# Kernel optimization log

Measured on AMD Instinct MI355X. Metric: run time of the kernel, lower is better.

Reference implementation:

```python
import jax, jax.numpy as jnp
import numpy as np

D_MODEL = 1024
N_HEADS = 16
D_H = D_MODEL // N_HEADS
B, S = 2, 2048


def setup_inputs() -> dict:
    key = jax.random.key(0)
    ks = jax.random.split(key, 12)
    s = 1.0 / np.sqrt(D_MODEL)
    inp = {
        "Q": jax.random.normal(ks[0], (B, S, D_MODEL), jnp.float32),
        "K": jax.random.normal(ks[1], (B, S, D_MODEL), jnp.float32),
        "V": jax.random.normal(ks[2], (B, S, D_MODEL), jnp.float32),
        # causal mask: True means masked out (matches masked_fill semantics)
        "masked": jnp.broadcast_to(~jnp.tril(jnp.ones((S, S), bool)), (B, S, S)),
        "WQ_w": jax.random.uniform(ks[3], (D_MODEL, D_MODEL), jnp.float32, -s, s),
        "WQ_b": jax.random.uniform(ks[4], (D_MODEL,), jnp.float32, -s, s),
        "WK_w": jax.random.uniform(ks[5], (D_MODEL, D_MODEL), jnp.float32, -s, s),
        "WK_b": jax.random.uniform(ks[6], (D_MODEL,), jnp.float32, -s, s),
        "WV_w": jax.random.uniform(ks[7], (D_MODEL, D_MODEL), jnp.float32, -s, s),
        "WV_b": jax.random.uniform(ks[8], (D_MODEL,), jnp.float32, -s, s),
        "Wo_w": jax.random.uniform(ks[9], (D_MODEL, D_MODEL), jnp.float32, -s, s),
        "Wo_b": jax.random.uniform(ks[10], (D_MODEL,), jnp.float32, -s, s),
    }
    return inp


def reference(Q, K, V, masked, WQ_w, WQ_b, WK_w, WK_b, WV_w, WV_b, Wo_w, Wo_b):
    b = Q.shape[0]
    # torch Linear: y = x @ W^T + b
    def split_heads(x):
        return x.reshape(b, -1, N_HEADS, D_H).transpose(0, 2, 1, 3)  # [B,H,S,d_h]

    q = split_heads(Q @ WQ_w.T + WQ_b)
    k = split_heads(K @ WK_w.T + WK_b)
    v = split_heads(V @ WV_w.T + WV_b)

    scores = jnp.einsum("bhqd,bhkd->bhqk", q, k) / np.sqrt(D_H)
    scores = jnp.where(masked[:, None, :, :], jnp.float32(-1e9), scores)
    attn = jax.nn.softmax(scores, axis=-1)
    ctx = jnp.einsum("bhqk,bhkd->bhqd", attn, v)  # [B,H,S,d_h]
    ctx = ctx.transpose(0, 2, 1, 3).reshape(b, -1, N_HEADS * D_H)
    return ctx @ Wo_w.T + Wo_b
```

## Files before the change

### kernel.cpp

```cpp
#include <hip/hip_runtime.h>
#include <hip/hip_bf16.h>
#include <math.h>


typedef __bf16 bf16_t;
typedef bf16_t bf16x8 __attribute__((ext_vector_type(8)));
typedef bf16_t bf16x4 __attribute__((ext_vector_type(4)));
typedef float f32x4 __attribute__((ext_vector_type(4)));

#define MFMA16(a, b, c) __builtin_amdgcn_mfma_f32_16x16x32_bf16(a, b, c, 0, 0, 0)

constexpr int S_LEN = 2048;
constexpr int DMODEL = 1024;
constexpr int DHEAD = 64;
constexpr int MTOT = 2 * S_LEN;
constexpr size_t NQ = (size_t)MTOT * DMODEL;
constexpr size_t NW = (size_t)DMODEL * DMODEL;
constexpr float ESC = 0.18033688011112042f;

__device__ __forceinline__ void load_lds16(const void* g, void* l) {
  __builtin_amdgcn_global_load_lds((const __attribute__((address_space(1))) void*)g,
                                   (__attribute__((address_space(3))) void*)l, 16, 0, 0);
}

__device__ __forceinline__ void swap32(unsigned& a, unsigned& b) {
#if __has_builtin(__builtin_amdgcn_permlane32_swap)
  auto r = __builtin_amdgcn_permlane32_swap(a, b, false, false);
  a = r[0]; b = r[1];
#else
  asm volatile("s_nop 1\n\tv_permlane32_swap_b32 %0, %1\n\ts_nop 1"
               : "+v"(a), "+v"(b));
#endif
}
__device__ __forceinline__ void swap16(unsigned& a, unsigned& b) {
#if __has_builtin(__builtin_amdgcn_permlane16_swap)
  auto r = __builtin_amdgcn_permlane16_swap(a, b, false, false);
  a = r[0]; b = r[1];
#else
  asm volatile("s_nop 1\n\tv_permlane16_swap_b32 %0, %1\n\ts_nop 1"
               : "+v"(a), "+v"(b));
#endif
}

__device__ __forceinline__ float fexp2(float x) {
#if __has_builtin(__builtin_amdgcn_exp2f)
  return __builtin_amdgcn_exp2f(x);
#else
  float r;
  asm("v_exp_f32 %0, %1\n\ts_nop 1" : "=v"(r) : "v"(x));
  return r;
#endif
}

__global__ __launch_bounds__(256) void convert_all(
    const float* __restrict__ Q, const float* __restrict__ K, const float* __restrict__ V,
    const float* __restrict__ W0, const float* __restrict__ W1, const float* __restrict__ W2,
    const float* __restrict__ W3, bf16_t* __restrict__ dst) {
  const size_t i = ((size_t)blockIdx.x * 256 + threadIdx.x) * 4;
  const float* s;
  size_t off = i;
  if (off < NQ) { s = Q; }
  else if (off < 2 * NQ) { s = K; off -= NQ; }
  else if (off < 3 * NQ) { s = V; off -= 2 * NQ; }
  else {
    off -= 3 * NQ;
    if (off < NW) { s = W0; }
    else if (off < 2 * NW) { s = W1; off -= NW; }
    else if (off < 3 * NW) { s = W2; off -= 2 * NW; }
    else { s = W3; off -= 3 * NW; }
  }
  const float4 v4 = *(const float4*)(s + off);
  bf16x4 b;
  b[0] = (bf16_t)v4.x; b[1] = (bf16_t)v4.y; b[2] = (bf16_t)v4.z; b[3] = (bf16_t)v4.w;
  *(bf16x4*)(dst + i) = b;
}

template <int BK>
__device__ __forceinline__ void gemm_loop(const bf16_t* __restrict__ Ab,
                                          const bf16_t* __restrict__ Wb,
                                          bf16_t* As, bf16_t* Ws,
                                          f32x4 (&acc)[4][4], int wave, int lane) {
  constexpr int CH = BK / 8;
  constexpr int RPI = 64 / CH;
  constexpr int IPW = BK / 16;
  const int col = lane & 15, quad = lane >> 4;
  const int wm = (wave >> 1) * 64, wn = (wave & 1) * 64;
  const int srow = lane / CH;
  const int sch = lane % CH;

  for (int k0 = 0; k0 < 1024; k0 += BK) {
    __syncthreads();
#pragma unroll
    for (int i = 0; i < IPW; i++) {
      const int rbase = (i * 4 + wave) * RPI;
      const int g = sch ^ ((rbase + srow) & 7);
      load_lds16(Ab + (size_t)(rbase + srow) * 1024 + k0 + g * 8, As + rbase * BK);
      load_lds16(Wb + (size_t)(rbase + srow) * 1024 + k0 + g * 8, Ws + rbase * BK);
    }
    __syncthreads();
#pragma unroll
    for (int kc = 0; kc < BK / 32; kc++) {
      const int slot = (kc * 4 + quad) ^ (col & 7);
      bf16x8 af[4], wf[4];
#pragma unroll
      for (int i = 0; i < 4; i++) af[i] = *(const bf16x8*)&As[(wm + i * 16 + col) * BK + slot * 8];
#pragma unroll
      for (int j = 0; j < 4; j++) wf[j] = *(const bf16x8*)&Ws[(wn + j * 16 + col) * BK + slot * 8];
#pragma unroll
      for (int i = 0; i < 4; i++)
#pragma unroll
        for (int j = 0; j < 4; j++) acc[i][j] = MFMA16(af[i], wf[j], acc[i][j]);
    }
  }
}

__global__ __launch_bounds__(256, 3) void gemm_qkv(const bf16_t* __restrict__ Abase,
                                                   const bf16_t* __restrict__ Wbase,
                                                   const float* __restrict__ b0,
                                                   const float* __restrict__ b1,
                                                   const float* __restrict__ b2,
                                                   bf16_t* __restrict__ obase) {
  __shared__ bf16_t As[128 * 64];
  __shared__ bf16_t Ws[128 * 64];
  const int z = blockIdx.z;
  const int bm = blockIdx.x * 128, bn = blockIdx.y * 128;
  const int lane = threadIdx.x & 63, wave = threadIdx.x >> 6;
  const int col = lane & 15, quad = lane >> 4;
  const int wm = (wave >> 1) * 64, wn = (wave & 1) * 64;

  f32x4 acc[4][4];
#pragma unroll
  for (int i = 0; i < 4; i++)
#pragma unroll
    for (int j = 0; j < 4; j++)
#pragma unroll
      for (int r = 0; r < 4; r++) acc[i][j][r] = 0.f;

  const bf16_t* A = Abase + z * NQ + (size_t)bm * 1024;
  const bf16_t* W = Wbase + z * NW + (size_t)bn * 1024;
  const float* bias = (z == 0) ? b0 : ((z == 1) ? b1 : b2);
  bf16_t* out = obase + z * NQ;

  gemm_loop<64>(A, W, As, Ws, acc, wave, lane);

  const float esc = (z == 0) ? ESC : 1.0f;
#pragma unroll
  for (int i = 0; i < 4; i++) {
#pragma unroll
    for (int j = 0; j < 4; j++) {
      const int n = bn + wn + j * 16 + col;
      const float bv = bias[n];
      const int h = n >> 6, dh = n & 63;
      if (z < 2) {
#pragma unroll
        for (int r = 0; r < 4; r++) {
          const int m = bm + wm + i * 16 + quad * 4 + r;
          const int b = m >> 11, s = m & 2047;
          out[((size_t)((b * 16 + h) * S_LEN + s) << 6) | dh] =
              (bf16_t)((acc[i][j][r] + bv) * esc);
        }
      } else {
        const int m0 = bm + wm + i * 16 + quad * 4;
        const int b = m0 >> 11, s0 = m0 & 2047;
        bf16x4 p4;
#pragma unroll
        for (int r = 0; r < 4; r++) p4[r] = (bf16_t)(acc[i][j][r] + bv);
        *(bf16x4*)&out[(((size_t)((b * 16 + h) * DHEAD + dh)) << 11) | s0] = p4;
      }
    }
  }
}

__global__ __launch_bounds__(256, 2) void gemm_out(const bf16_t* __restrict__ A,
                                                   const bf16_t* __restrict__ W,
                                                   const float* __restrict__ bias,
                                                   float* __restrict__ out) {
  __shared__ bf16_t As[64 * 64];
  __shared__ bf16_t Ws[128 * 64];
  const int bm = blockIdx.x * 64, bn = blockIdx.y * 128;
  const int lane = threadIdx.x & 63, wave = threadIdx.x >> 6;
  const int col = lane & 15, quad = lane >> 4;
  const int wm = (wave >> 1) * 32, wn = (wave & 1) * 64;

  f32x4 acc[2][4];
#pragma unroll
  for (int i = 0; i < 2; i++)
#pragma unroll
    for (int j = 0; j < 4; j++)
#pragma unroll
      for (int r = 0; r < 4; r++) acc[i][j][r] = 0.f;

  const int srow = lane >> 3, s7 = lane & 7;
  const bf16_t* Ab = A + (size_t)bm * 1024;
  const bf16_t* Wb = W + (size_t)bn * 1024;

  for (int k0 = 0; k0 < 1024; k0 += 64) {
    __syncthreads();
#pragma unroll
    for (int i = 0; i < 2; i++) {
      const int rbase = (i * 4 + wave) * 8;
      const int g = s7 ^ srow;
      load_lds16(Ab + (size_t)(rbase + srow) * 1024 + k0 + g * 8, As + rbase * 64);
    }
#pragma unroll
    for (int i = 0; i < 4; i++) {
      const int rbase = (i * 4 + wave) * 8;
      const int g = s7 ^ srow;
      load_lds16(Wb + (size_t)(rbase + srow) * 1024 + k0 + g * 8, Ws + rbase * 64);
    }
    __syncthreads();
#pragma unroll
    for (int kc = 0; kc < 2; kc++) {
      const int slot = (kc * 4 + quad) ^ (col & 7);
      bf16x8 af[2], wf[4];
#pragma unroll
      for (int i = 0; i < 2; i++) af[i] = *(const bf16x8*)&As[(wm + i * 16 + col) * 64 + slot * 8];
#pragma unroll
      for (int j = 0; j < 4; j++) wf[j] = *(const bf16x8*)&Ws[(wn + j * 16 + col) * 64 + slot * 8];
#pragma unroll
      for (int i = 0; i < 2; i++)
#pragma unroll
        for (int j = 0; j < 4; j++) acc[i][j] = MFMA16(af[i], wf[j], acc[i][j]);
    }
  }

#pragma unroll
  for (int i = 0; i < 2; i++)
#pragma unroll
    for (int j = 0; j < 4; j++) {
      const int n = bn + wn + j * 16 + col;
      const float bv = bias[n];
#pragma unroll
      for (int r = 0; r < 4; r++) {
        const int m = bm + wm + i * 16 + quad * 4 + r;
        out[(size_t)m * DMODEL + n] = acc[i][j][r] + bv;
      }
    }
}

__global__ __launch_bounds__(256, 2) void attn(const bf16_t* __restrict__ q,
                                               const bf16_t* __restrict__ k,
                                               const bf16_t* __restrict__ vT,
                                               bf16_t* __restrict__ ctx) {
  const int bh = blockIdx.x;
  const int y = blockIdx.y;
  const int T = (y < 8) ? (15 - y) : (y - 8);
  const int cmax = 2 * T + 1;
  const int lane = threadIdx.x & 63, wave = threadIdx.x >> 6;
  const int col = lane & 15, quad = lane >> 4;
  const int qrel = wave * 16 + col;

  __shared__ bf16_t Ks[2][64 * 64];
  __shared__ bf16_t Vs[2][64 * 64];

  const bf16_t* kbh = k + (size_t)bh * S_LEN * DHEAD;
  const bf16_t* vbh = vT + (size_t)bh * DHEAD * S_LEN;

  const int srow8 = lane >> 3, s7 = lane & 7;
  const int g8 = s7 ^ srow8;

  auto stage = [&](int c, int b) {
#pragma unroll
    for (int i = 0; i < 2; i++) {
      const int rbase = (i * 4 + wave) * 8;
      load_lds16(kbh + (size_t)(c * 64 + rbase + srow8) * DHEAD + g8 * 8,
                 &Ks[b][rbase * 64]);
    }
#pragma unroll
    for (int i = 0; i < 2; i++) {
      const int dbase = (i * 4 + wave) * 8;
      load_lds16(vbh + (size_t)(dbase + srow8) * S_LEN + c * 64 + g8 * 8,
                 &Vs[b][dbase * 64]);
    }
  };

  const bf16_t* qb0 = q + ((size_t)bh * S_LEN + T * 128 + qrel) * DHEAD;
  bf16x8 aq[2][2];
  aq[0][0] = *(const bf16x8*)(qb0 + quad * 8);
  aq[0][1] = *(const bf16x8*)(qb0 + 32 + quad * 8);
  aq[1][0] = *(const bf16x8*)(qb0 + (size_t)64 * DHEAD + quad * 8);
  aq[1][1] = *(const bf16x8*)(qb0 + (size_t)64 * DHEAD + 32 + quad * 8);

  f32x4 o0[4], o1[4], lacc0, lacc1;
#pragma unroll
  for (int db = 0; db < 4; db++)
#pragma unroll
    for (int r = 0; r < 4; r++) { o0[db][r] = 0.f; o1[db][r] = 0.f; }
#pragma unroll
  for (int r = 0; r < 4; r++) { lacc0[r] = 0.f; lacc1[r] = 0.f; }
  const f32x4 Zv = {0.f, 0.f, 0.f, 0.f};

  auto expw = [&](const f32x4& sv, int nb, bool dmask, f32x4& lac,
                  unsigned& w0, unsigned& w1) {
    union { bf16x4 v; unsigned u[2]; } pw;
#pragma unroll
    for (int r = 0; r < 4; r++) {
      float pv = fexp2(sv[r]);
      if (dmask && (nb * 16 + quad * 4 + r) > qrel) pv = 0.f;
      lac[r] += pv;
      pw.v[r] = (bf16_t)pv;
    }
    w0 = pw.u[0]; w1 = pw.u[1];
  };

  stage(0, 0);
  int buf = 0;

  for (int c = 0; c <= cmax; ++c) {
    __syncthreads();
    if (c < cmax) stage(c + 1, buf ^ 1);

    const bool skip0 = (c == cmax);
    const bool mask0 = (c == cmax - 1);
    const bool mask1 = (c == cmax);

    f32x4 s0[4], s1[4];
    {
      const int sl = quad ^ (col & 7);
      bf16x8 kf[4];
#pragma unroll
      for (int nb = 0; nb < 4; nb++)
        kf[nb] = *(const bf16x8*)&Ks[buf][(nb * 16 + col) * 64 + sl * 8];
      __builtin_amdgcn_s_setprio(1);
      if (!skip0) {
#pragma unroll
        for (int nb = 0; nb < 4; nb++) s0[nb] = MFMA16(kf[nb], aq[0][0], Zv);
      }
#pragma unroll
      for (int nb = 0; nb < 4; nb++) s1[nb] = MFMA16(kf[nb], aq[1][0], Zv);
      __builtin_amdgcn_s_setprio(0);
    }
    {
      const int sl = (4 + quad) ^ (col & 7);
      bf16x8 kf[4];
#pragma unroll
      for (int nb = 0; nb < 4; nb++)
        kf[nb] = *(const bf16x8*)&Ks[buf][(nb * 16 + col) * 64 + sl * 8];
      __builtin_amdgcn_s_setprio(1);
      if (!skip0) {
#pragma unroll
        for (int nb = 0; nb < 4; nb++) s0[nb] = MFMA16(kf[nb], aq[0][1], s0[nb]);
      }
#pragma unroll
      for (int nb = 0; nb < 4; nb++) s1[nb] = MFMA16(kf[nb], aq[1][1], s1[nb]);
      __builtin_amdgcn_s_setprio(0);
    }

#pragma unroll
    for (int kcp = 0; kcp < 2; kcp++) {
      const int sl = (kcp * 4 + quad) ^ (col & 7);
      bf16x8 bv[4];
#pragma unroll
      for (int db = 0; db < 4; db++)
        bv[db] = *(const bf16x8*)&Vs[buf][(db * 16 + col) * 64 + sl * 8];

      union { unsigned u[4]; bf16x8 v; } pa1, pa0;
      {
        unsigned X0, X1, Y0, Y1;
        expw(s1[2 * kcp], 2 * kcp, mask1, lacc1, X0, X1);
        expw(s1[2 * kcp + 1], 2 * kcp + 1, mask1, lacc1, Y0, Y1);
        swap32(X0, Y0); swap16(X0, Y0);
        swap32(X1, Y1); swap16(X1, Y1);
        pa1.u[0] = X0; pa1.u[1] = X1; pa1.u[2] = Y0; pa1.u[3] = Y1;
      }
      if (!skip0) {
        unsigned X0, X1, Y0, Y1;
        expw(s0[2 * kcp], 2 * kcp, mask0, lacc0, X0, X1);
        expw(s0[2 * kcp + 1], 2 * kcp + 1, mask0, lacc0, Y0, Y1);
        swap32(X0, Y0); swap16(X0, Y0);
        swap32(X1, Y1); swap16(X1, Y1);
        pa0.u[0] = X0; pa0.u[1] = X1; pa0.u[2] = Y0; pa0.u[3] = Y1;
      }
      __builtin_amdgcn_s_setprio(1);
      if (!skip0) {
#pragma unroll
        for (int db = 0; db < 4; db++) o0[db] = MFMA16(bv[db], pa0.v, o0[db]);
      }
#pragma unroll
      for (int db = 0; db < 4; db++) o1[db] = MFMA16(bv[db], pa1.v, o1[db]);
      __builtin_amdgcn_s_setprio(0);
    }
    buf ^= 1;
  }

  float l0 = lacc0[0] + lacc0[1] + lacc0[2] + lacc0[3];
  l0 += __shfl_xor(l0, 16); l0 += __shfl_xor(l0, 32);
  float l1 = lacc1[0] + lacc1[1] + lacc1[2] + lacc1[3];
  l1 += __shfl_xor(l1, 16); l1 += __shfl_xor(l1, 32);
  const float inv0 = 1.f / l0, inv1 = 1.f / l1;
  const int b = bh >> 4, h = bh & 15;
  bf16_t* cb0 = ctx + ((size_t)(b * S_LEN + T * 128 + qrel)) * DMODEL + h * DHEAD;
  bf16_t* cb1 = cb0 + (size_t)64 * DMODEL;
#pragma unroll
  for (int db = 0; db < 4; db++) {
    bf16x4 w0, w1;
#pragma unroll
    for (int r = 0; r < 4; r++) {
      w0[r] = (bf16_t)(o0[db][r] * inv0);
      w1[r] = (bf16_t)(o1[db][r] * inv1);
    }
    *(bf16x4*)&cb0[db * 16 + quad * 4] = w0;
    *(bf16x4*)&cb1[db * 16 + quad * 4] = w1;
  }
}

extern "C" void kernel_launch(void* const* d_in, const int* in_sizes, int n_in,
                              void* d_out, int out_size, void* d_ws, size_t ws_size,
                              hipStream_t stream) {
  const float* Q = (const float*)d_in[0];
  const float* K = (const float*)d_in[1];
  const float* V = (const float*)d_in[2];
  const float* WQw = (const float*)d_in[4];
  const float* WQb = (const float*)d_in[5];
  const float* WKw = (const float*)d_in[6];
  const float* WKb = (const float*)d_in[7];
  const float* WVw = (const float*)d_in[8];
  const float* WVb = (const float*)d_in[9];
  const float* Wow = (const float*)d_in[10];
  const float* Wob = (const float*)d_in[11];

  bf16_t* base = (bf16_t*)d_ws;
  bf16_t* Wc = base + 3 * NQ;
  bf16_t* qp = base + 3 * NQ + 4 * NW;
  bf16_t* ctx = base;

  const size_t total = 3 * NQ + 4 * NW;
  convert_all<<<dim3((unsigned)(total / 4 / 256)), dim3(256), 0, stream>>>(
      Q, K, V, WQw, WKw, WVw, Wow, base);

  gemm_qkv<<<dim3(32, 8, 3), dim3(256), 0, stream>>>(base, Wc, WQb, WKb, WVb, qp);
  attn<<<dim3(32, 16), dim3(256), 0, stream>>>(qp, qp + NQ, qp + 2 * NQ, ctx);
  gemm_out<<<dim3(64, 8), dim3(256), 0, stream>>>(ctx, Wc + 3 * NW, Wob, (float*)d_out);
}
```

Baseline: 233.9 us.

## Balance causal attention by pairing query tiles and splitting across two blocks

```diff
diff --git a/kernel.cpp b/kernel.cpp
--- a/kernel.cpp
+++ b/kernel.cpp
@@ -241,11 +241,15 @@
 __global__ __launch_bounds__(256, 2) void attn(const bf16_t* __restrict__ q,
                                                const bf16_t* __restrict__ k,
                                                const bf16_t* __restrict__ vT,
-                                               bf16_t* __restrict__ ctx) {
+                                               bf16_t* __restrict__ ctx,
+                                               float* __restrict__ pO,
+                                               float* __restrict__ pL) {
   const int bh = blockIdx.x;
-  const int y = blockIdx.y;
-  const int T = (y < 8) ? (15 - y) : (y - 8);
-  const int cmax = 2 * T + 1;
+  const int p = blockIdx.y;
+  const int s = blockIdx.z;
+  const int tB = 15 - p;
+  const int nA = s ? 0 : (2 * p + 2);
+  const int cB0 = s ? (15 - 2 * p) : 0;
   const int lane = threadIdx.x & 63, wave = threadIdx.x >> 6;
   const int col = lane & 15, quad = lane >> 4;
   const int qrel = wave * 16 + col;
@@ -274,20 +278,8 @@
     }
   };
 
-  const bf16_t* qb0 = q + ((size_t)bh * S_LEN + T * 128 + qrel) * DHEAD;
-  bf16x8 aq[2][2];
-  aq[0][0] = *(const bf16x8*)(qb0 + quad * 8);
-  aq[0][1] = *(const bf16x8*)(qb0 + 32 + quad * 8);
-  aq[1][0] = *(const bf16x8*)(qb0 + (size_t)64 * DHEAD + quad * 8);
-  aq[1][1] = *(const bf16x8*)(qb0 + (size_t)64 * DHEAD + 32 + quad * 8);
-
+  bf16x8 aqw[2][2];
   f32x4 o0[4], o1[4], lacc0, lacc1;
-#pragma unroll
-  for (int db = 0; db < 4; db++)
-#pragma unroll
-    for (int r = 0; r < 4; r++) { o0[db][r] = 0.f; o1[db][r] = 0.f; }
-#pragma unroll
-  for (int r = 0; r < 4; r++) { lacc0[r] = 0.f; lacc1[r] = 0.f; }
   const f32x4 Zv = {0.f, 0.f, 0.f, 0.f};
 
   auto expw = [&](const f32x4& sv, int nb, bool dmask, f32x4& lac,
@@ -303,16 +295,41 @@
     w0 = pw.u[0]; w1 = pw.u[1];
   };
 
-  stage(0, 0);
+  stage(cB0, 0);
   int buf = 0;
 
-  for (int c = 0; c <= cmax; ++c) {
+#pragma unroll 1
+  for (int i = 0; i < 17; ++i) {
+    const bool inB = (i >= nA);
+    const int c = inB ? (cB0 + i - nA) : i;
+    const int cm = inB ? (2 * tB + 1) : (2 * p + 1);
+
+    if (i == 0 || i == nA) {
+      const int tq = inB ? tB : p;
+      const bf16_t* qb = q + ((size_t)bh * S_LEN + tq * 128 + qrel) * DHEAD;
+      aqw[0][0] = *(const bf16x8*)(qb + quad * 8);
+      aqw[0][1] = *(const bf16x8*)(qb + 32 + quad * 8);
+      aqw[1][0] = *(const bf16x8*)(qb + (size_t)64 * DHEAD + quad * 8);
+      aqw[1][1] = *(const bf16x8*)(qb + (size_t)64 * DHEAD + 32 + quad * 8);
+#pragma unroll
+      for (int r = 0; r < 4; r++) { lacc0[r] = 0.f; lacc1[r] = 0.f; }
+#pragma unroll
+      for (int db = 0; db < 4; db++)
+#pragma unroll
+        for (int r = 0; r < 4; r++) { o0[db][r] = 0.f; o1[db][r] = 0.f; }
+    }
+
     __syncthreads();
-    if (c < cmax) stage(c + 1, buf ^ 1);
-
-    const bool skip0 = (c == cmax);
-    const bool mask0 = (c == cmax - 1);
-    const bool mask1 = (c == cmax);
+
+    if (i < 16) {
+      const int i1 = i + 1;
+      const int c1 = (i1 < nA) ? i1 : (cB0 + i1 - nA);
+      stage(c1, buf ^ 1);
+    }
+
+    const bool skip0 = (c == cm);
+    const bool mask0 = (c == cm - 1);
+    const bool mask1 = (c == cm);
 
     f32x4 s0[4], s1[4];
     {
@@ -324,10 +341,10 @@
       __builtin_amdgcn_s_setprio(1);
       if (!skip0) {
 #pragma unroll
-        for (int nb = 0; nb < 4; nb++) s0[nb] = MFMA16(kf[nb], aq[0][0], Zv);
-      }
-#pragma unroll
-      for (int nb = 0; nb < 4; nb++) s1[nb] = MFMA16(kf[nb], aq[1][0], Zv);
+        for (int nb = 0; nb < 4; nb++) s0[nb] = MFMA16(kf[nb], aqw[0][0], Zv);
+      }
+#pragma unroll
+      for (int nb = 0; nb < 4; nb++) s1[nb] = MFMA16(kf[nb], aqw[1][0], Zv);
       __builtin_amdgcn_s_setprio(0);
     }
     {
@@ -339,10 +356,10 @@
       __builtin_amdgcn_s_setprio(1);
       if (!skip0) {
 #pragma unroll
-        for (int nb = 0; nb < 4; nb++) s0[nb] = MFMA16(kf[nb], aq[0][1], s0[nb]);
-      }
-#pragma unroll
-      for (int nb = 0; nb < 4; nb++) s1[nb] = MFMA16(kf[nb], aq[1][1], s1[nb]);
+        for (int nb = 0; nb < 4; nb++) s0[nb] = MFMA16(kf[nb], aqw[0][1], s0[nb]);
+      }
+#pragma unroll
+      for (int nb = 0; nb < 4; nb++) s1[nb] = MFMA16(kf[nb], aqw[1][1], s1[nb]);
       __builtin_amdgcn_s_setprio(0);
     }
 
@@ -380,6 +397,28 @@
       for (int db = 0; db < 4; db++) o1[db] = MFMA16(bv[db], pa1.v, o1[db]);
       __builtin_amdgcn_s_setprio(0);
     }
+
+    if (i == nA - 1) {
+      float l0 = lacc0[0] + lacc0[1] + lacc0[2] + lacc0[3];
+      l0 += __shfl_xor(l0, 16); l0 += __shfl_xor(l0, 32);
+      float l1 = lacc1[0] + lacc1[1] + lacc1[2] + lacc1[3];
+      l1 += __shfl_xor(l1, 16); l1 += __shfl_xor(l1, 32);
+      const float inv0 = 1.f / l0, inv1 = 1.f / l1;
+      const int b = bh >> 4, h = bh & 15;
+      bf16_t* cb0 = ctx + ((size_t)(b * S_LEN + p * 128 + qrel)) * DMODEL + h * DHEAD;
+      bf16_t* cb1 = cb0 + (size_t)64 * DMODEL;
+#pragma unroll
+      for (int db = 0; db < 4; db++) {
+        bf16x4 w0, w1;
+#pragma unroll
+        for (int r = 0; r < 4; r++) {
+          w0[r] = (bf16_t)(o0[db][r] * inv0);
+          w1[r] = (bf16_t)(o1[db][r] * inv1);
+        }
+        *(bf16x4*)&cb0[db * 16 + quad * 4] = w0;
+        *(bf16x4*)&cb1[db * 16 + quad * 4] = w1;
+      }
+    }
     buf ^= 1;
   }
 
@@ -387,20 +426,39 @@
   l0 += __shfl_xor(l0, 16); l0 += __shfl_xor(l0, 32);
   float l1 = lacc1[0] + lacc1[1] + lacc1[2] + lacc1[3];
   l1 += __shfl_xor(l1, 16); l1 += __shfl_xor(l1, 32);
-  const float inv0 = 1.f / l0, inv1 = 1.f / l1;
+  const int slot = ((bh * 8 + p) << 1) | s;
+  float* myO = pO + (size_t)slot * (128 * 64);
+  float* myL = pL + slot * 128;
+#pragma unroll
+  for (int db = 0; db < 4; db++) {
+    *(f32x4*)&myO[(size_t)qrel * 64 + db * 16 + quad * 4] = o0[db];
+    *(f32x4*)&myO[(size_t)(64 + qrel) * 64 + db * 16 + quad * 4] = o1[db];
+  }
+  if (quad == 0) { myL[qrel] = l0; myL[64 + qrel] = l1; }
+}
+
+__global__ __launch_bounds__(256) void combine(const float* __restrict__ pO,
+                                               const float* __restrict__ pL,
+                                               bf16_t* __restrict__ ctx) {
+  const int pair = blockIdx.x;
+  const int bh = pair >> 3, p = pair & 7;
+  const int tB = 15 - p;
   const int b = bh >> 4, h = bh & 15;
-  bf16_t* cb0 = ctx + ((size_t)(b * S_LEN + T * 128 + qrel)) * DMODEL + h * DHEAD;
-  bf16_t* cb1 = cb0 + (size_t)64 * DMODEL;
-#pragma unroll
-  for (int db = 0; db < 4; db++) {
-    bf16x4 w0, w1;
-#pragma unroll
-    for (int r = 0; r < 4; r++) {
-      w0[r] = (bf16_t)(o0[db][r] * inv0);
-      w1[r] = (bf16_t)(o1[db][r] * inv1);
-    }
-    *(bf16x4*)&cb0[db * 16 + quad * 4] = w0;
-    *(bf16x4*)&cb1[db * 16 + quad * 4] = w1;
+  const float* O0 = pO + (size_t)(pair * 2 + 0) * (128 * 64);
+  const float* O1 = pO + (size_t)(pair * 2 + 1) * (128 * 64);
+  const float* L0 = pL + (pair * 2 + 0) * 128;
+  const float* L1 = pL + (pair * 2 + 1) * 128;
+#pragma unroll
+  for (int n = 0; n < 8; n++) {
+    const int idx = n * 1024 + threadIdx.x * 4;
+    const int r = idx >> 6, cdh = idx & 63;
+    const f32x4 a = *(const f32x4*)&O0[idx];
+    const f32x4 c4 = *(const f32x4*)&O1[idx];
+    const float inv = 1.f / (L0[r] + L1[r]);
+    bf16x4 w;
+#pragma unroll
+    for (int j = 0; j < 4; j++) w[j] = (bf16_t)((a[j] + c4[j]) * inv);
+    *(bf16x4*)&ctx[((size_t)(b * S_LEN + tB * 128 + r)) * DMODEL + h * DHEAD + cdh] = w;
   }
 }
 
@@ -423,12 +481,15 @@
   bf16_t* Wc = base + 3 * NQ;
   bf16_t* qp = base + 3 * NQ + 4 * NW;
   bf16_t* ctx = base;
+  float* pO = (float*)(base + NQ);
+  float* pL = (float*)(base + 3 * NQ);
 
   const size_t total = 3 * NQ + 4 * NW;
   convert_all<<<dim3((unsigned)(total / 4 / 256)), dim3(256), 0, stream>>>(
       Q, K, V, WQw, WKw, WVw, Wow, base);
 
   gemm_qkv<<<dim3(32, 8, 3), dim3(256), 0, stream>>>(base, Wc, WQb, WKb, WVb, qp);
-  attn<<<dim3(32, 16), dim3(256), 0, stream>>>(qp, qp + NQ, qp + 2 * NQ, ctx);
+  attn<<<dim3(32, 8, 2), dim3(256), 0, stream>>>(qp, qp + NQ, qp + 2 * NQ, ctx, pO, pL);
+  combine<<<dim3(256), dim3(256), 0, stream>>>(pO, pL, ctx);
   gemm_out<<<dim3(64, 8), dim3(256), 0, stream>>>(ctx, Wc + 3 * NW, Wob, (float*)d_out);
 }
```

Result: faster. 225.5 us (-3.6%).
